# Performance work log

Measured on AMD Instinct MI355X. Metric: run time of the kernel, lower is better.

Reference implementation:

```python
import jax, jax.numpy as jnp
import numpy as np

NV, NJ, NB_POSE = 778, 16, 135
PARENTS = np.array([-1, 0, 1, 2, 0, 4, 5, 0, 7, 8, 0, 10, 11, 0, 13, 14], dtype=np.int32)
FINGER_IDX = np.array([734, 333, 443, 555, 678], dtype=np.int32)


def setup_inputs() -> dict:
    key = jax.random.key(0)
    ks = jax.random.split(key, 9)
    B = 4096
    return {
        "beta": jax.random.normal(ks[0], (B, 10), jnp.float32) * 0.3,
        "theta": jax.random.normal(ks[1], (B, 48), jnp.float32) * 0.3,
        "v_template": jax.random.normal(ks[2], (NV, 3), jnp.float32) * 0.05,
        "shapedirs": jax.random.normal(ks[3], (10, NV * 3), jnp.float32) * 0.01,
        "posedirs": jax.random.normal(ks[4], (NB_POSE, NV * 3), jnp.float32) * 0.01,
        "J_regressor": jax.random.uniform(ks[5], (NV, NJ), jnp.float32) / NV,
        "weights": jax.random.uniform(ks[6], (NV, NJ), jnp.float32),
        "hands_mean": jax.random.normal(ks[7], (45,), jnp.float32) * 0.1,
        "hands_components": jax.random.normal(ks[8], (45, 45), jnp.float32) * 0.1,
    }


def batch_rodrigues(r):
    """Axis-angle [N,3] -> rotation matrices [N,3,3] (Rodrigues formula)."""
    eps = 1e-8
    angle = jnp.linalg.norm(r + eps, axis=1, keepdims=True)          # [N,1]
    axis = r / angle
    x, y, z = axis[:, 0], axis[:, 1], axis[:, 2]
    zeros = jnp.zeros_like(x)
    K = jnp.stack([zeros, -z, y, z, zeros, -x, -y, x, zeros], axis=1).reshape(-1, 3, 3)
    a = angle[:, :, None]                                            # [N,1,1]
    I3 = jnp.eye(3, dtype=r.dtype)
    return I3 + jnp.sin(a) * K + (1.0 - jnp.cos(a)) * (K @ K)


def global_rigid_transform(Rs, Js):
    """Rs [B,16,3,3], Js [B,16,3] -> relative skinning transforms A [B,16,4,4]."""
    B = Rs.shape[0]
    bot = jnp.broadcast_to(jnp.array([0.0, 0.0, 0.0, 1.0], Rs.dtype), (B, 1, 4))

    def make_A(R, t):  # R [B,3,3], t [B,3] -> [B,4,4]
        return jnp.concatenate([jnp.concatenate([R, t[:, :, None]], axis=2), bot], axis=1)

    results = [make_A(Rs[:, 0], Js[:, 0])]
    for i in range(1, NJ):  # fixed small kinematic chain
        t = Js[:, i] - Js[:, PARENTS[i]]
        results.append(results[PARENTS[i]] @ make_A(Rs[:, i], t))
    res = jnp.stack(results, axis=1)                                 # [B,16,4,4]
    Js_h = jnp.concatenate([Js, jnp.zeros((B, NJ, 1), Rs.dtype)], axis=2)  # [B,16,4]
    init_bone = jnp.einsum('bjpq,bjq->bjp', res, Js_h)               # [B,16,4]
    return res.at[:, :, :, 3].add(-init_bone)                        # A = res - pack(res @ [J;0])


def reference(beta, theta, v_template, shapedirs, posedirs, J_regressor, weights,
              hands_mean, hands_components):
    B = beta.shape[0]
    P = theta.shape[1] - 3
    # full pose: global rot + PCA-recovered local rotations
    full_local = theta[:, 3:] @ hands_components[:P, :] + hands_mean  # [B,45]
    pose = jnp.concatenate([theta[:, :3], full_local], axis=1)       # [B,48]

    # shape blend
    v_shaped = (beta @ shapedirs).reshape(B, NV, 3) + v_template     # [B,778,3]
    J = jnp.einsum('bvc,vj->bjc', v_shaped, J_regressor)             # [B,16,3]

    # pose blend
    Rs = batch_rodrigues(pose.reshape(-1, 3)).reshape(B, NJ, 3, 3)
    pose_feature = (Rs[:, 1:] - jnp.eye(3, dtype=Rs.dtype)).reshape(B, NB_POSE)
    v_posed = (pose_feature @ posedirs).reshape(B, NV, 3) + v_shaped

    # kinematic chain + linear blend skinning
    A = global_rigid_transform(Rs, J)                                # [B,16,4,4]
    T = jnp.einsum('vj,bjpq->bvpq', weights, A)                      # [B,778,4,4]
    v_homo = jnp.concatenate([v_posed, jnp.ones((B, NV, 1), v_posed.dtype)], axis=2)
    verts = jnp.einsum('bvpq,bvq->bvp', T, v_homo)[:, :, :3]         # [B,778,3]

    joints = jnp.einsum('bvc,vj->bjc', verts, J_regressor)           # [B,16,3]
    joints = jnp.concatenate([joints, verts[:, FINGER_IDX, :]], axis=1)  # [B,21,3]
    return joints
```

## Files before the change

### kernel.cpp

```cpp
#include <hip/hip_runtime.h>

#define NV  778
#define NBP 135
#define NK  146
#define NKQ 152
#define GC  4
#define VCH 49

#define FV0 734
#define FV1 333
#define FV2 443
#define FV3 555
#define FV4 678

__device__ __forceinline__ const float* d_row(int k,
                                              const float* vt,
                                              const float* sd,
                                              const float* pd) {
    return (k == 0) ? vt : (k <= 10 ? sd + (size_t)(k-1)*(NV*3)
                                    : pd + (size_t)(k-11)*(NV*3));
}

__launch_bounds__(256)
__global__ void k_fold(const float* __restrict__ vt,
                       const float* __restrict__ sd,
                       const float* __restrict__ pd,
                       const float* __restrict__ jreg,
                       const float* __restrict__ wts,
                       float* __restrict__ SJ, float* __restrict__ JT,
                       float* __restrict__ WJ, float* __restrict__ Gq,
                       float* __restrict__ Dfing, float* __restrict__ Wfing)
{
    const int o = blockIdx.x;
    const int tid = threadIdx.x;

    if (o < 2336) {
        const int k = o >> 4, chunk = o & 15;
        const int J = tid >> 4, j = tid & 15;
        const float* Drow = d_row(k, vt, sd, pd);
        const int v0 = chunk * VCH;
        const int v1 = (v0 + VCH < NV) ? (v0 + VCH) : NV;
        float a0 = 0.f, a1 = 0.f, a2 = 0.f;
        #pragma unroll 7
        for (int v = v0; v < v1; ++v) {
            float pv = jreg[v*16 + J] * wts[v*16 + j];
            a0 += Drow[3*v+0] * pv;
            a1 += Drow[3*v+1] * pv;
            a2 += Drow[3*v+2] * pv;
        }
        float* gp = Gq + ((size_t)k*256 + tid)*3;
        atomicAdd(gp+0, a0);
        atomicAdd(gp+1, a1);
        atomicAdd(gp+2, a2);
    } else if (o < 2468) {
        const int idx = (o - 2336)*4 + (tid >> 6);
        const int t = tid & 63;
        const float* src; int jc;
        if (idx < 480) { int k = idx / 48; jc = idx % 48; src = sd + (size_t)k*(NV*3); }
        else           { jc = idx - 480;              src = vt; }
        int j = jc / 3, c = jc % 3;
        float acc = 0.f;
        for (int v = t; v < NV; v += 64)
            acc += src[3*v + c] * jreg[v*16 + j];
        for (int off = 32; off; off >>= 1) acc += __shfl_down(acc, off, 64);
        if (t == 0) { if (idx < 480) SJ[idx] = acc; else JT[jc] = acc; }
    } else if (o < 2532) {
        const int cidx = (o - 2468)*4 + (tid >> 6);
        const int t = tid & 63;
        const int J = cidx >> 4, j = cidx & 15;
        float acc = 0.f;
        for (int v = t; v < NV; v += 64)
            acc += jreg[v*16 + J] * wts[v*16 + j];
        for (int off = 32; off; off >>= 1) acc += __shfl_down(acc, off, 64);
        if (t == 0) WJ[cidx] = acc;
    } else {
        const int fv[5] = {FV0, FV1, FV2, FV3, FV4};
        for (int e = tid; e < NK*15; e += 256) {
            int k = e / 15, r = e % 15, f = r / 3, q = r % 3;
            Dfing[e] = d_row(k, vt, sd, pd)[3*fv[f] + q];
        }
        if (tid < 80) {
            int f = tid >> 4, j = tid & 15;
            Wfing[tid] = wts[fv[f]*16 + j];
        }
    }
}

__launch_bounds__(256)
__global__ void kC(const float* __restrict__ beta,
                   const float* __restrict__ theta,
                   const float* __restrict__ hm,
                   const float* __restrict__ hc,
                   const float* __restrict__ SJ,
                   const float* __restrict__ JT,
                   const float* __restrict__ WJ,
                   const float* __restrict__ Gq,
                   const float* __restrict__ Dfing,
                   const float* __restrict__ Wfing,
                   float* __restrict__ out,
                   int Btot)
{
    const int tid = threadIdx.x;
    const int w = tid >> 6, t = tid & 63;
    const int b0 = blockIdx.x * GC;

    __shared__ float s_SJ[480];
    __shared__ float s_JT[48];
    __shared__ float s_WJ[256];
    __shared__ float s_beta[GC][10];
    __shared__ __align__(16) float s_coef[GC][152];
    __shared__ float s_A[GC][192];
    __shared__ float s_vpf[GC][16];
    __shared__ __align__(16) char s_un[3177*4];
    float* s_S    = (float*)s_un;
    float* u_hc   = (float*)s_un;
    float* u_th   = u_hc + 2025;
    float* u_pose = u_th + GC*48;
    float* u_J    = u_pose + GC*48;
    float* u_R    = u_J + GC*48;

    float cur0[8], cur1[8], cur2[8];
    #pragma unroll
    for (int kk = 0; kk < 8; ++kk) {
        const float* gq = Gq + ((size_t)kk*256 + tid)*3;
        cur0[kk] = gq[0]; cur1[kk] = gq[1]; cur2[kk] = gq[2];
    }

    for (int i = tid; i < 2025; i += 256) u_hc[i] = hc[i];
    for (int i = tid; i < 480;  i += 256) s_SJ[i] = SJ[i];
    if (tid < 48) s_JT[tid] = JT[tid];
    s_WJ[tid] = WJ[tid];
    for (int i = tid; i < GC*48; i += 256) {
        int g = i / 48, tt = i % 48, b = b0 + g;
        u_th[g*48 + tt] = (b < Btot) ? theta[(size_t)b*48 + tt] : 0.f;
    }
    for (int i = tid; i < GC*10; i += 256) {
        int g = i / 10, k = i % 10, b = b0 + g;
        s_beta[g][k] = (b < Btot) ? beta[(size_t)b*10 + k] : 0.f;
    }
    for (int i = tid; i < GC*152; i += 256) ((float*)s_coef)[i] = 0.f;
    __syncthreads();

    {
        const int g = w;
        const int b = b0 + g;
        if (b < Btot) {
            float* pose = u_pose + g*48;
            float* Jg   = u_J + g*48;
            float* Rg   = u_R + g*144;
            const float* th = u_th + g*48;
            if (t < 3) pose[t] = th[t];
            if (t < 45) {
                float acc = hm[t];
                #pragma unroll 9
                for (int k = 0; k < 45; ++k) acc += th[3+k] * u_hc[k*45 + t];
                pose[3+t] = acc;
            }
            if (t < 48) {
                float acc = s_JT[t];
                #pragma unroll
                for (int k = 0; k < 10; ++k) acc += s_beta[g][k] * s_SJ[k*48 + t];
                Jg[t] = acc;
            }
            if (t < 10) s_coef[g][1+t] = s_beta[g][t];
            if (t == 10) s_coef[g][0] = 1.f;
            if (t < 16) {
                float rx = pose[3*t], ry = pose[3*t+1], rz = pose[3*t+2];
                float ex = rx + 1e-8f, ey = ry + 1e-8f, ez = rz + 1e-8f;
                float angle = sqrtf(ex*ex + ey*ey + ez*ez);
                float inv = 1.f / angle;
                float x = rx*inv, y = ry*inv, z = rz*inv;
                float s  = sinf(angle);
                float c1 = 1.f - cosf(angle);
                float R[9];
                R[0] = 1.f + c1*(-(z*z + y*y));
                R[1] = -s*z + c1*(x*y);
                R[2] =  s*y + c1*(x*z);
                R[3] =  s*z + c1*(x*y);
                R[4] = 1.f + c1*(-(x*x + z*z));
                R[5] = -s*x + c1*(y*z);
                R[6] = -s*y + c1*(x*z);
                R[7] =  s*x + c1*(y*z);
                R[8] = 1.f + c1*(-(x*x + y*y));
                #pragma unroll
                for (int i = 0; i < 9; ++i) Rg[t*9 + i] = R[i];
                if (t >= 1) {
                    #pragma unroll
                    for (int i = 0; i < 9; ++i)
                        s_coef[g][11 + (t-1)*9 + i] = R[i] - ((i % 4 == 0) ? 1.f : 0.f);
                }
            }
            if (t < 16) {
                float res[12];
                #pragma unroll
                for (int p = 0; p < 3; ++p) {
                    res[p*4+0] = Rg[p*3+0];
                    res[p*4+1] = Rg[p*3+1];
                    res[p*4+2] = Rg[p*3+2];
                    res[p*4+3] = Jg[p];
                }
                if (t >= 1) {
                    int start = ((t-1)/3)*3 + 1;
                    int d = t - start;
                    for (int s = 0; s < 3; ++s) {
                        if (s <= d) {
                            int a  = start + s;
                            int pa = (s == 0) ? 0 : (a - 1);
                            float ax = Jg[a*3+0] - Jg[pa*3+0];
                            float ay = Jg[a*3+1] - Jg[pa*3+1];
                            float az = Jg[a*3+2] - Jg[pa*3+2];
                            float nr[12];
                            #pragma unroll
                            for (int p = 0; p < 3; ++p) {
                                float r0 = res[p*4+0], r1 = res[p*4+1], r2 = res[p*4+2];
                                #pragma unroll
                                for (int q = 0; q < 3; ++q)
                                    nr[p*4+q] = r0*Rg[a*9+q] + r1*Rg[a*9+3+q] + r2*Rg[a*9+6+q];
                                nr[p*4+3] = r0*ax + r1*ay + r2*az + res[p*4+3];
                            }
                            #pragma unroll
                            for (int q = 0; q < 12; ++q) res[q] = nr[q];
                        }
                    }
                }
                float jx = Jg[t*3+0], jy = Jg[t*3+1], jz = Jg[t*3+2];
                #pragma unroll
                for (int p = 0; p < 3; ++p) {
                    float r0 = res[p*4+0], r1 = res[p*4+1], r2 = res[p*4+2];
                    float ib = r0*jx + r1*jy + r2*jz;
                    s_A[g][t*12 + p*4+0] = r0;
                    s_A[g][t*12 + p*4+1] = r1;
                    s_A[g][t*12 + p*4+2] = r2;
                    s_A[g][t*12 + p*4+3] = res[p*4+3] - ib;
                }
            }
        }
    }
    __syncthreads();

    {
        float acc[GC][3];
        #pragma unroll
        for (int g = 0; g < GC; ++g) { acc[g][0]=0.f; acc[g][1]=0.f; acc[g][2]=0.f; }
        for (int k = 0; k < NKQ; k += 8) {
            float nxt0[8], nxt1[8], nxt2[8];
            if (k + 8 < NKQ) {
                #pragma unroll
                for (int kk = 0; kk < 8; ++kk) {
                    const float* gq = Gq + ((size_t)(k+8+kk)*256 + tid)*3;
                    nxt0[kk] = gq[0]; nxt1[kk] = gq[1]; nxt2[kk] = gq[2];
                }
            }
            #pragma unroll
            for (int g = 0; g < GC; ++g) {
                float4 cA = *(const float4*)&s_coef[g][k];
                float4 cB = *(const float4*)&s_coef[g][k+4];
                float cf[8] = {cA.x,cA.y,cA.z,cA.w, cB.x,cB.y,cB.z,cB.w};
                #pragma unroll
                for (int kk = 0; kk < 8; ++kk) {
                    acc[g][0] += cf[kk]*cur0[kk];
                    acc[g][1] += cf[kk]*cur1[kk];
                    acc[g][2] += cf[kk]*cur2[kk];
                }
            }
            if (k + 8 < NKQ) {
                #pragma unroll
                for (int kk = 0; kk < 8; ++kk) {
                    cur0[kk] = nxt0[kk]; cur1[kk] = nxt1[kk]; cur2[kk] = nxt2[kk];
                }
            }
        }
        __syncthreads();
        #pragma unroll
        for (int g = 0; g < GC; ++g) {
            s_S[g*768 + tid*3 + 0] = acc[g][0];
            s_S[g*768 + tid*3 + 1] = acc[g][1];
            s_S[g*768 + tid*3 + 2] = acc[g][2];
        }
    }
    __syncthreads();

    if (tid < GC*48) {
        int g = tid / 48, rem = tid % 48, J = rem / 3, p = rem % 3;
        int b = b0 + g;
        if (b < Btot) {
            const float* Ag = s_A[g];
            const float* Sg = s_S + g*768 + J*48;
            float val = 0.f;
            #pragma unroll
            for (int j = 0; j < 16; ++j) {
                val += Ag[j*12 + p*4 + 0] * Sg[j*3+0]
                     + Ag[j*12 + p*4 + 1] * Sg[j*3+1]
                     + Ag[j*12 + p*4 + 2] * Sg[j*3+2]
                     + Ag[j*12 + p*4 + 3] * s_WJ[J*16 + j];
            }
            out[(size_t)b*63 + J*3 + p] = val;
        }
    }

    if (tid >= 192 && tid < 192 + GC*15) {
        int r2 = tid - 192;
        int g = r2 / 15, r = r2 % 15;
        float acc = 0.f;
        #pragma unroll 4
        for (int k = 0; k < NK; ++k) acc += s_coef[g][k] * Dfing[k*15 + r];
        s_vpf[g][r] = acc;
    }
    __syncthreads();
    if (tid >= 192 && tid < 192 + GC*15) {
        int r2 = tid - 192;
        int g = r2 / 15, r = r2 % 15, f = r / 3, p = r % 3;
        int b = b0 + g;
        if (b < Btot) {
            const float* Ag = s_A[g];
            float vx = s_vpf[g][f*3+0], vy = s_vpf[g][f*3+1], vz = s_vpf[g][f*3+2];
            float val = 0.f;
            #pragma unroll
            for (int j = 0; j < 16; ++j) {
                float wj = Wfing[f*16 + j];
                val += wj * (Ag[j*12 + p*4 + 0]*vx +
                             Ag[j*12 + p*4 + 1]*vy +
                             Ag[j*12 + p*4 + 2]*vz +
                             Ag[j*12 + p*4 + 3]);
            }
            out[(size_t)b*63 + (16+f)*3 + p] = val;
        }
    }
}

extern "C" void kernel_launch(void* const* d_in, const int* in_sizes, int n_in,
                              void* d_out, int out_size, void* d_ws, size_t ws_size,
                              hipStream_t stream) {
    const float* beta       = (const float*)d_in[0];
    const float* theta      = (const float*)d_in[1];
    const float* v_template = (const float*)d_in[2];
    const float* shapedirs  = (const float*)d_in[3];
    const float* posedirs   = (const float*)d_in[4];
    const float* J_reg      = (const float*)d_in[5];
    const float* weights    = (const float*)d_in[6];
    const float* hands_mean = (const float*)d_in[7];
    const float* hands_comp = (const float*)d_in[8];
    float* out = (float*)d_out;

    const int B = in_sizes[0] / 10;

    float* W = (float*)d_ws;
    float* SJ    = W;
    float* JT    = W + 480;
    float* WJ    = W + 528;
    float* Dfing = W + 784;
    float* Wfing = W + 2974;
    float* Gq    = W + 3072;

    hipMemsetAsync(Gq, 0, (size_t)NKQ*768*sizeof(float), stream);
    k_fold<<<2533, 256, 0, stream>>>(v_template, shapedirs, posedirs, J_reg, weights,
                                     SJ, JT, WJ, Gq, Dfing, Wfing);
    kC<<<(B + GC - 1)/GC, 256, 0, stream>>>(beta, theta, hands_mean, hands_comp,
                                            SJ, JT, WJ, Gq, Dfing, Wfing, out, B);
}
```

Before: 137.8 us.

## Move pose/Rodrigues precompute into fold kernel and use shuffle-reduced joint output

The per-sample PCA pose recovery and Rodrigues rotations now run in extra blocks of the fold kernel and write coefficient vectors and root rotations to global workspace. The main kernel drops from four to two samples per block and rebuilds rotation matrices from the stored coefficients. The joint output is reduced with wave shuffles instead of staging through shared memory, and the finger dot product is split across eight partial sums. This lowers per-block shared memory and serial setup work in the main kernel, at the cost of a global round-trip for the coefficients, twice as many main-kernel blocks, and each block reading the whole Gq table to serve half as many samples.

```diff
diff --git a/kernel.cpp b/kernel.cpp
--- a/kernel.cpp
+++ b/kernel.cpp
@@ -4,7 +4,7 @@
 #define NBP 135
 #define NK  146
 #define NKQ 152
-#define GC  4
+#define GC  2
 #define VCH 49
 
 #define FV0 734
@@ -27,12 +27,22 @@
                        const float* __restrict__ pd,
                        const float* __restrict__ jreg,
                        const float* __restrict__ wts,
+                       const float* __restrict__ beta,
+                       const float* __restrict__ theta,
+                       const float* __restrict__ hm,
+                       const float* __restrict__ hc,
                        float* __restrict__ SJ, float* __restrict__ JT,
                        float* __restrict__ WJ, float* __restrict__ Gq,
-                       float* __restrict__ Dfing, float* __restrict__ Wfing)
+                       float* __restrict__ coefG, float* __restrict__ R0G,
+                       float* __restrict__ Dfing, float* __restrict__ Wfing,
+                       int Btot, int npb)
 {
     const int o = blockIdx.x;
     const int tid = threadIdx.x;
+
+    __shared__ float p_hc[2025];
+    __shared__ float p_th[8][48];
+    __shared__ float p_pose[8][45];
 
     if (o < 2336) {
         const int k = o >> 4, chunk = o & 15;
@@ -73,99 +83,29 @@
             acc += jreg[v*16 + J] * wts[v*16 + j];
         for (int off = 32; off; off >>= 1) acc += __shfl_down(acc, off, 64);
         if (t == 0) WJ[cidx] = acc;
-    } else {
-        const int fv[5] = {FV0, FV1, FV2, FV3, FV4};
-        for (int e = tid; e < NK*15; e += 256) {
-            int k = e / 15, r = e % 15, f = r / 3, q = r % 3;
-            Dfing[e] = d_row(k, vt, sd, pd)[3*fv[f] + q];
-        }
-        if (tid < 80) {
-            int f = tid >> 4, j = tid & 15;
-            Wfing[tid] = wts[fv[f]*16 + j];
-        }
-    }
-}
-
-__launch_bounds__(256)
-__global__ void kC(const float* __restrict__ beta,
-                   const float* __restrict__ theta,
-                   const float* __restrict__ hm,
-                   const float* __restrict__ hc,
-                   const float* __restrict__ SJ,
-                   const float* __restrict__ JT,
-                   const float* __restrict__ WJ,
-                   const float* __restrict__ Gq,
-                   const float* __restrict__ Dfing,
-                   const float* __restrict__ Wfing,
-                   float* __restrict__ out,
-                   int Btot)
-{
-    const int tid = threadIdx.x;
-    const int w = tid >> 6, t = tid & 63;
-    const int b0 = blockIdx.x * GC;
-
-    __shared__ float s_SJ[480];
-    __shared__ float s_JT[48];
-    __shared__ float s_WJ[256];
-    __shared__ float s_beta[GC][10];
-    __shared__ __align__(16) float s_coef[GC][152];
-    __shared__ float s_A[GC][192];
-    __shared__ float s_vpf[GC][16];
-    __shared__ __align__(16) char s_un[3177*4];
-    float* s_S    = (float*)s_un;
-    float* u_hc   = (float*)s_un;
-    float* u_th   = u_hc + 2025;
-    float* u_pose = u_th + GC*48;
-    float* u_J    = u_pose + GC*48;
-    float* u_R    = u_J + GC*48;
-
-    float cur0[8], cur1[8], cur2[8];
-    #pragma unroll
-    for (int kk = 0; kk < 8; ++kk) {
-        const float* gq = Gq + ((size_t)kk*256 + tid)*3;
-        cur0[kk] = gq[0]; cur1[kk] = gq[1]; cur2[kk] = gq[2];
-    }
-
-    for (int i = tid; i < 2025; i += 256) u_hc[i] = hc[i];
-    for (int i = tid; i < 480;  i += 256) s_SJ[i] = SJ[i];
-    if (tid < 48) s_JT[tid] = JT[tid];
-    s_WJ[tid] = WJ[tid];
-    for (int i = tid; i < GC*48; i += 256) {
-        int g = i / 48, tt = i % 48, b = b0 + g;
-        u_th[g*48 + tt] = (b < Btot) ? theta[(size_t)b*48 + tt] : 0.f;
-    }
-    for (int i = tid; i < GC*10; i += 256) {
-        int g = i / 10, k = i % 10, b = b0 + g;
-        s_beta[g][k] = (b < Btot) ? beta[(size_t)b*10 + k] : 0.f;
-    }
-    for (int i = tid; i < GC*152; i += 256) ((float*)s_coef)[i] = 0.f;
-    __syncthreads();
-
-    {
-        const int g = w;
-        const int b = b0 + g;
-        if (b < Btot) {
-            float* pose = u_pose + g*48;
-            float* Jg   = u_J + g*48;
-            float* Rg   = u_R + g*144;
-            const float* th = u_th + g*48;
-            if (t < 3) pose[t] = th[t];
-            if (t < 45) {
-                float acc = hm[t];
-                #pragma unroll 9
-                for (int k = 0; k < 45; ++k) acc += th[3+k] * u_hc[k*45 + t];
-                pose[3+t] = acc;
-            }
-            if (t < 48) {
-                float acc = s_JT[t];
-                #pragma unroll
-                for (int k = 0; k < 10; ++k) acc += s_beta[g][k] * s_SJ[k*48 + t];
-                Jg[t] = acc;
-            }
-            if (t < 10) s_coef[g][1+t] = s_beta[g][t];
-            if (t == 10) s_coef[g][0] = 1.f;
-            if (t < 16) {
-                float rx = pose[3*t], ry = pose[3*t+1], rz = pose[3*t+2];
+    } else if (o < 2532 + npb) {
+        const int b0 = (o - 2532) * 8;
+        for (int i = tid; i < 2025; i += 256) p_hc[i] = hc[i];
+        for (int i = tid; i < 8*48; i += 256) {
+            int g = i / 48, t = i % 48, b = b0 + g;
+            p_th[g][t] = (b < Btot) ? theta[(size_t)b*48 + t] : 0.f;
+        }
+        __syncthreads();
+        for (int i = tid; i < 8*45; i += 256) {
+            int g = i / 45, t = i % 45;
+            float acc = hm[t];
+            #pragma unroll 9
+            for (int k = 0; k < 45; ++k) acc += p_th[g][3+k] * p_hc[k*45 + t];
+            p_pose[g][t] = acc;
+        }
+        __syncthreads();
+        if (tid < 128) {
+            int g = tid >> 4, jt = tid & 15;
+            int b = b0 + g;
+            if (b < Btot) {
+                float rx, ry, rz;
+                if (jt == 0) { rx = p_th[g][0]; ry = p_th[g][1]; rz = p_th[g][2]; }
+                else { rx = p_pose[g][3*(jt-1)+0]; ry = p_pose[g][3*(jt-1)+1]; rz = p_pose[g][3*(jt-1)+2]; }
                 float ex = rx + 1e-8f, ey = ry + 1e-8f, ez = rz + 1e-8f;
                 float angle = sqrtf(ex*ex + ey*ey + ez*ez);
                 float inv = 1.f / angle;
@@ -182,21 +122,99 @@
                 R[6] = -s*y + c1*(x*z);
                 R[7] =  s*x + c1*(y*z);
                 R[8] = 1.f + c1*(-(x*x + y*y));
-                #pragma unroll
-                for (int i = 0; i < 9; ++i) Rg[t*9 + i] = R[i];
-                if (t >= 1) {
+                float* cg = coefG + (size_t)b*152;
+                if (jt == 0) {
+                    #pragma unroll
+                    for (int i = 0; i < 9; ++i) R0G[(size_t)b*9 + i] = R[i];
+                    cg[0] = 1.f;
+                    #pragma unroll
+                    for (int k = 0; k < 10; ++k) cg[1+k] = beta[(size_t)b*10 + k];
+                    #pragma unroll
+                    for (int k = 146; k < 152; ++k) cg[k] = 0.f;
+                } else {
                     #pragma unroll
                     for (int i = 0; i < 9; ++i)
-                        s_coef[g][11 + (t-1)*9 + i] = R[i] - ((i % 4 == 0) ? 1.f : 0.f);
+                        cg[11 + (jt-1)*9 + i] = R[i] - ((i % 4 == 0) ? 1.f : 0.f);
                 }
             }
+        }
+    } else {
+        const int fv[5] = {FV0, FV1, FV2, FV3, FV4};
+        for (int e = tid; e < NK*15; e += 256) {
+            int k = e / 15, r = e % 15, f = r / 3, q = r % 3;
+            Dfing[e] = d_row(k, vt, sd, pd)[3*fv[f] + q];
+        }
+        if (tid < 80) {
+            int f = tid >> 4, j = tid & 15;
+            Wfing[tid] = wts[fv[f]*16 + j];
+        }
+    }
+}
+
+__launch_bounds__(256)
+__global__ void kC(const float* __restrict__ SJ,
+                   const float* __restrict__ JT,
+                   const float* __restrict__ WJ,
+                   const float* __restrict__ Gq,
+                   const float* __restrict__ coefG,
+                   const float* __restrict__ R0G,
+                   const float* __restrict__ Dfing,
+                   const float* __restrict__ Wfing,
+                   float* __restrict__ out,
+                   int Btot)
+{
+    const int tid = threadIdx.x;
+    const int w = tid >> 6, t = tid & 63;
+    const int b0 = blockIdx.x * GC;
+
+    __shared__ float s_SJ[480];
+    __shared__ float s_JT[48];
+    __shared__ float s_WJ[256];
+    __shared__ __align__(16) float s_coef[GC][152];
+    __shared__ float s_R0[GC][9];
+    __shared__ float s_A[GC][192];
+    __shared__ float s_J[GC][48];
+    __shared__ float s_vpf[GC][16];
+    __shared__ float s_fred[GC][15][8];
+
+    float cur0[8], cur1[8], cur2[8];
+    #pragma unroll
+    for (int kk = 0; kk < 8; ++kk) {
+        const float* gq = Gq + ((size_t)kk*256 + tid)*3;
+        cur0[kk] = gq[0]; cur1[kk] = gq[1]; cur2[kk] = gq[2];
+    }
+
+    for (int i = tid; i < 480; i += 256) s_SJ[i] = SJ[i];
+    if (tid < 48) s_JT[tid] = JT[tid];
+    s_WJ[tid] = WJ[tid];
+    for (int i = tid; i < GC*152; i += 256) {
+        int g = i / 152, k = i % 152, b = b0 + g;
+        s_coef[g][k] = (b < Btot) ? coefG[(size_t)b*152 + k] : 0.f;
+    }
+    if (tid < GC*9) {
+        int g = tid / 9, i = tid % 9, b = b0 + g;
+        s_R0[g][i] = (b < Btot) ? R0G[(size_t)b*9 + i] : 0.f;
+    }
+    __syncthreads();
+
+    if (w < GC) {
+        const int g = w;
+        const int b = b0 + g;
+        if (b < Btot) {
+            if (t < 48) {
+                float acc = s_JT[t];
+                #pragma unroll
+                for (int k = 0; k < 10; ++k) acc += s_coef[g][1+k] * s_SJ[k*48 + t];
+                s_J[g][t] = acc;
+            }
             if (t < 16) {
+                float* Jg = s_J[g];
                 float res[12];
                 #pragma unroll
                 for (int p = 0; p < 3; ++p) {
-                    res[p*4+0] = Rg[p*3+0];
-                    res[p*4+1] = Rg[p*3+1];
-                    res[p*4+2] = Rg[p*3+2];
+                    res[p*4+0] = s_R0[g][p*3+0];
+                    res[p*4+1] = s_R0[g][p*3+1];
+                    res[p*4+2] = s_R0[g][p*3+2];
                     res[p*4+3] = Jg[p];
                 }
                 if (t >= 1) {
@@ -206,6 +224,11 @@
                         if (s <= d) {
                             int a  = start + s;
                             int pa = (s == 0) ? 0 : (a - 1);
+                            const float* cr = &s_coef[g][11 + (a-1)*9];
+                            float Ra[9];
+                            #pragma unroll
+                            for (int i = 0; i < 9; ++i)
+                                Ra[i] = cr[i] + ((i % 4 == 0) ? 1.f : 0.f);
                             float ax = Jg[a*3+0] - Jg[pa*3+0];
                             float ay = Jg[a*3+1] - Jg[pa*3+1];
                             float az = Jg[a*3+2] - Jg[pa*3+2];
@@ -215,7 +238,7 @@
                                 float r0 = res[p*4+0], r1 = res[p*4+1], r2 = res[p*4+2];
                                 #pragma unroll
                                 for (int q = 0; q < 3; ++q)
-                                    nr[p*4+q] = r0*Rg[a*9+q] + r1*Rg[a*9+3+q] + r2*Rg[a*9+6+q];
+                                    nr[p*4+q] = r0*Ra[q] + r1*Ra[3+q] + r2*Ra[6+q];
                                 nr[p*4+3] = r0*ax + r1*ay + r2*az + res[p*4+3];
                             }
                             #pragma unroll
@@ -238,78 +261,77 @@
     }
     __syncthreads();
 
-    {
-        float acc[GC][3];
-        #pragma unroll
-        for (int g = 0; g < GC; ++g) { acc[g][0]=0.f; acc[g][1]=0.f; acc[g][2]=0.f; }
-        for (int k = 0; k < NKQ; k += 8) {
-            float nxt0[8], nxt1[8], nxt2[8];
-            if (k + 8 < NKQ) {
-                #pragma unroll
-                for (int kk = 0; kk < 8; ++kk) {
-                    const float* gq = Gq + ((size_t)(k+8+kk)*256 + tid)*3;
-                    nxt0[kk] = gq[0]; nxt1[kk] = gq[1]; nxt2[kk] = gq[2];
-                }
-            }
-            #pragma unroll
-            for (int g = 0; g < GC; ++g) {
-                float4 cA = *(const float4*)&s_coef[g][k];
-                float4 cB = *(const float4*)&s_coef[g][k+4];
-                float cf[8] = {cA.x,cA.y,cA.z,cA.w, cB.x,cB.y,cB.z,cB.w};
-                #pragma unroll
-                for (int kk = 0; kk < 8; ++kk) {
-                    acc[g][0] += cf[kk]*cur0[kk];
-                    acc[g][1] += cf[kk]*cur1[kk];
-                    acc[g][2] += cf[kk]*cur2[kk];
-                }
-            }
-            if (k + 8 < NKQ) {
-                #pragma unroll
-                for (int kk = 0; kk < 8; ++kk) {
-                    cur0[kk] = nxt0[kk]; cur1[kk] = nxt1[kk]; cur2[kk] = nxt2[kk];
-                }
-            }
-        }
-        __syncthreads();
+    float acc[GC][3];
+    #pragma unroll
+    for (int g = 0; g < GC; ++g) { acc[g][0]=0.f; acc[g][1]=0.f; acc[g][2]=0.f; }
+    for (int k = 0; k < NKQ; k += 8) {
+        float nxt0[8], nxt1[8], nxt2[8];
+        if (k + 8 < NKQ) {
+            #pragma unroll
+            for (int kk = 0; kk < 8; ++kk) {
+                const float* gq = Gq + ((size_t)(k+8+kk)*256 + tid)*3;
+                nxt0[kk] = gq[0]; nxt1[kk] = gq[1]; nxt2[kk] = gq[2];
+            }
+        }
         #pragma unroll
         for (int g = 0; g < GC; ++g) {
-            s_S[g*768 + tid*3 + 0] = acc[g][0];
-            s_S[g*768 + tid*3 + 1] = acc[g][1];
-            s_S[g*768 + tid*3 + 2] = acc[g][2];
-        }
+            float4 cA = *(const float4*)&s_coef[g][k];
+            float4 cB = *(const float4*)&s_coef[g][k+4];
+            float cf[8] = {cA.x,cA.y,cA.z,cA.w, cB.x,cB.y,cB.z,cB.w};
+            #pragma unroll
+            for (int kk = 0; kk < 8; ++kk) {
+                acc[g][0] += cf[kk]*cur0[kk];
+                acc[g][1] += cf[kk]*cur1[kk];
+                acc[g][2] += cf[kk]*cur2[kk];
+            }
+        }
+        if (k + 8 < NKQ) {
+            #pragma unroll
+            for (int kk = 0; kk < 8; ++kk) {
+                cur0[kk] = nxt0[kk]; cur1[kk] = nxt1[kk]; cur2[kk] = nxt2[kk];
+            }
+        }
+    }
+
+    {
+        const int J = tid >> 4, j = tid & 15;
+        #pragma unroll
+        for (int g = 0; g < GC; ++g) {
+            const float* Aj = &s_A[g][j*12];
+            float wj = s_WJ[J*16 + j];
+            float v0 = Aj[0]*acc[g][0] + Aj[1]*acc[g][1] + Aj[2]*acc[g][2]  + Aj[3]*wj;
+            float v1 = Aj[4]*acc[g][0] + Aj[5]*acc[g][1] + Aj[6]*acc[g][2]  + Aj[7]*wj;
+            float v2 = Aj[8]*acc[g][0] + Aj[9]*acc[g][1] + Aj[10]*acc[g][2] + Aj[11]*wj;
+            #pragma unroll
+            for (int off = 1; off < 16; off <<= 1) {
+                v0 += __shfl_xor(v0, off, 64);
+                v1 += __shfl_xor(v1, off, 64);
+                v2 += __shfl_xor(v2, off, 64);
+            }
+            int b = b0 + g;
+            if (j == 0 && b < Btot) {
+                float* ob = out + (size_t)b*63 + J*3;
+                ob[0] = v0; ob[1] = v1; ob[2] = v2;
+            }
+        }
+    }
+
+    if (tid < GC*120) {
+        int g = tid / 120, rem = tid % 120, sl = rem / 15, r = rem % 15;
+        int k0 = sl*19, k1 = (k0+19 < NK) ? k0+19 : NK;
+        float a = 0.f;
+        for (int k = k0; k < k1; ++k) a += s_coef[g][k] * Dfing[k*15 + r];
+        s_fred[g][r][sl] = a;
     }
     __syncthreads();
-
-    if (tid < GC*48) {
-        int g = tid / 48, rem = tid % 48, J = rem / 3, p = rem % 3;
-        int b = b0 + g;
-        if (b < Btot) {
-            const float* Ag = s_A[g];
-            const float* Sg = s_S + g*768 + J*48;
-            float val = 0.f;
-            #pragma unroll
-            for (int j = 0; j < 16; ++j) {
-                val += Ag[j*12 + p*4 + 0] * Sg[j*3+0]
-                     + Ag[j*12 + p*4 + 1] * Sg[j*3+1]
-                     + Ag[j*12 + p*4 + 2] * Sg[j*3+2]
-                     + Ag[j*12 + p*4 + 3] * s_WJ[J*16 + j];
-            }
-            out[(size_t)b*63 + J*3 + p] = val;
-        }
-    }
-
-    if (tid >= 192 && tid < 192 + GC*15) {
-        int r2 = tid - 192;
-        int g = r2 / 15, r = r2 % 15;
-        float acc = 0.f;
-        #pragma unroll 4
-        for (int k = 0; k < NK; ++k) acc += s_coef[g][k] * Dfing[k*15 + r];
-        s_vpf[g][r] = acc;
+    if (tid < GC*15) {
+        int g = tid / 15, r = tid % 15;
+        const float* fr = s_fred[g][r];
+        s_vpf[g][r] = fr[0]+fr[1]+fr[2]+fr[3]+fr[4]+fr[5]+fr[6]+fr[7];
     }
     __syncthreads();
-    if (tid >= 192 && tid < 192 + GC*15) {
-        int r2 = tid - 192;
-        int g = r2 / 15, r = r2 % 15, f = r / 3, p = r % 3;
+    if (tid < GC*15) {
+        int g = tid / 15, r = tid % 15, f = r / 3, p = r % 3;
         int b = b0 + g;
         if (b < Btot) {
             const float* Ag = s_A[g];
@@ -343,6 +365,7 @@
     float* out = (float*)d_out;
 
     const int B = in_sizes[0] / 10;
+    const int npb = (B + 7) / 8;
 
     float* W = (float*)d_ws;
     float* SJ    = W;
@@ -351,10 +374,14 @@
     float* Dfing = W + 784;
     float* Wfing = W + 2974;
     float* Gq    = W + 3072;
+    float* coefG = W + 119808;
+    float* R0G   = coefG + (size_t)B*152;
 
     hipMemsetAsync(Gq, 0, (size_t)NKQ*768*sizeof(float), stream);
-    k_fold<<<2533, 256, 0, stream>>>(v_template, shapedirs, posedirs, J_reg, weights,
-                                     SJ, JT, WJ, Gq, Dfing, Wfing);
-    kC<<<(B + GC - 1)/GC, 256, 0, stream>>>(beta, theta, hands_mean, hands_comp,
-                                            SJ, JT, WJ, Gq, Dfing, Wfing, out, B);
+    k_fold<<<2533 + npb, 256, 0, stream>>>(v_template, shapedirs, posedirs, J_reg,
+                                           weights, beta, theta, hands_mean, hands_comp,
+                                           SJ, JT, WJ, Gq, coefG, R0G, Dfing, Wfing,
+                                           B, npb);
+    kC<<<(B + GC - 1)/GC, 256, 0, stream>>>(SJ, JT, WJ, Gq, coefG, R0G,
+                                            Dfing, Wfing, out, B);
 }
```

Result: slower. 147.6 us (+7.1%).
